# Kernel optimization log

Hardware: AMD Instinct MI355X
Metric: run time of the kernel (lower is better)

Reference implementation:

```python
import math
import jax, jax.numpy as jnp
import numpy as np

C = 1024  # n_embd
B, T = 4, 2048
H = 4 * C  # mlp hidden
EPS = 1e-5


def setup_inputs() -> dict:
    key = jax.random.key(0)
    ks = jax.random.split(key, 8)
    s = 0.02
    return {
        "x": jax.random.normal(ks[0], (B, T, C), jnp.float32),
        "ln1_g": jnp.ones((C,), jnp.float32),
        "ln1_b": jnp.zeros((C,), jnp.float32),
        "w_attn": jax.random.normal(ks[1], (C, 3 * C), jnp.float32) * s,
        "b_attn": jnp.zeros((3 * C,), jnp.float32),
        "w_proj": jax.random.normal(ks[2], (C, C), jnp.float32) * s,
        "b_proj": jnp.zeros((C,), jnp.float32),
        "ln2_g": jnp.ones((C,), jnp.float32),
        "ln2_b": jnp.zeros((C,), jnp.float32),
        "w_fc": jax.random.normal(ks[3], (C, H), jnp.float32) * s,
        "b_fc": jnp.zeros((H,), jnp.float32),
        "w_mlp_proj": jax.random.normal(ks[4], (H, C), jnp.float32) * s,
        "b_mlp_proj": jnp.zeros((C,), jnp.float32),
    }


def _layernorm(x, g, b):
    mu = jnp.mean(x, axis=-1, keepdims=True)
    var = jnp.mean(jnp.square(x - mu), axis=-1, keepdims=True)
    return (x - mu) * jax.lax.rsqrt(var + EPS) * g + b


def _new_gelu(x):
    c = math.sqrt(2.0 / math.pi)
    return 0.5 * x * (1.0 + jnp.tanh(c * (x + 0.044715 * x * x * x)))


def reference(x, ln1_g, ln1_b, w_attn, b_attn, w_proj, b_proj,
              ln2_g, ln2_b, w_fc, b_fc, w_mlp_proj, b_mlp_proj):
    # --- attention sublayer (single-head, full-dim, no causal mask) ---
    h = _layernorm(x, ln1_g, ln1_b)
    qkv = h @ w_attn + b_attn              # [B,T,3C]
    q, k, v = jnp.split(qkv, 3, axis=-1)   # each [B,T,C]
    scale = 1.0 / math.sqrt(C)
    att = jnp.einsum("btc,bsc->bts", q, k) * scale  # [B,T,T]
    att = jax.nn.softmax(att, axis=-1)
    y = jnp.einsum("bts,bsc->btc", att, v)
    y = y @ w_proj + b_proj
    x = x + y
    # --- MLP sublayer ---
    h2 = _layernorm(x, ln2_g, ln2_b)
    m = _new_gelu(h2 @ w_fc + b_fc) @ w_mlp_proj + b_mlp_proj
    return x + m
```

## Files before the change

kernel.cpp:

```cpp
#include <hip/hip_runtime.h>

typedef __bf16 bf16;
typedef bf16 bf16x8 __attribute__((ext_vector_type(8)));
typedef bf16 bf16x4 __attribute__((ext_vector_type(4)));
typedef float f32x4 __attribute__((ext_vector_type(4)));

#define C_DIM 1024
#define T_DIM 2048
#define B_DIM 4
#define H_DIM 4096

__device__ inline void gld_lds16(const bf16* g, bf16* l) {
    __builtin_amdgcn_global_load_lds(
        (const __attribute__((address_space(1))) unsigned int*)g,
        (__attribute__((address_space(3))) unsigned int*)l,
        16, 0, 0);
}

__device__ inline float fast_gelu(float u) {
    float k2 = 1.5957691216057308f * u + 0.07135480895843475f * u * u * u;
    float t = __expf(-k2);
    return u * __builtin_amdgcn_rcpf(1.0f + t);
}

template <int EPI, typename OutT, int BN>
__launch_bounds__(512, 2)
__global__ void gemm8p(const bf16* __restrict__ A, int lda, long long sA,
                       const bf16* __restrict__ Bt, int ldb, long long sB,
                       OutT* __restrict__ Cout, int ldc, long long sC,
                       const float* __restrict__ bias,
                       const float* __restrict__ resid, long long sR,
                       float alpha, int K) {
    constexpr int FN = BN / 64;
    constexpr int BQ = BN / 128;

    const int z = blockIdx.z;
    A += (long long)z * sA;
    Bt += (long long)z * sB;
    Cout += (long long)z * sC;
    if (resid) resid += (long long)z * sR;

    const int rowBase = blockIdx.x * 256;
    const int colBase = blockIdx.y * BN;

    __shared__ __align__(16) bf16 As[2 * 2 * 256 * 32];
    __shared__ __align__(16) bf16 Bs[2 * 2 * BN * 32];

    const int tid = threadIdx.x;
    const int w = tid >> 6;
    const int lane = tid & 63;
    const int wm = w >> 2, wn = w & 3;
    const int lr = lane & 15, lc = lane >> 4;

    const bf16* Ag = A + (size_t)(rowBase + (tid >> 2)) * lda + (tid & 3) * 8;
    const bf16* Bg = Bt + (size_t)(colBase + (tid >> 2)) * ldb + (tid & 3) * 8;
    const size_t ldaL = (size_t)lda, ldbL = (size_t)ldb;
    bf16* AsW = As + w * 512;
    bf16* BsW = Bs + w * 512;

    const int aBase = wm * 4096 + lr * 32 + lc * 8;
    const int bBase = wn * (FN * 512) + lr * 32 + lc * 8;

#define STAGE_A(buf, ks, tau) do {                                         \
        const bf16* _g = Ag + (size_t)(tau) * 64 + (ks) * 32;              \
        bf16* _l = AsW + ((buf) * 2 + (ks)) * 8192;                        \
        gld_lds16(_g, _l);                                                 \
        gld_lds16(_g + 128 * ldaL, _l + 4096);                             \
    } while (0)

#define STAGE_B(buf, ks, tau) do {                                         \
        const bf16* _g = Bg + (size_t)(tau) * 64 + (ks) * 32;              \
        bf16* _l = BsW + ((buf) * 2 + (ks)) * (BN * 32);                   \
        gld_lds16(_g, _l);                                                 \
        if constexpr (BQ == 2) gld_lds16(_g + 128 * ldbL, _l + 4096);      \
    } while (0)

#define LOAD_A(buf, ks, rh) do {                                           \
        _Pragma("unroll")                                                  \
        for (int i = 0; i < 4; i++)                                        \
            af[i] = *(const bf16x8*)(As + aBase + ((buf) * 2 + (ks)) * 8192 \
                                     + (rh) * 2048 + i * 512);             \
    } while (0)

#define LOAD_B(dst, buf, ks) do {                                          \
        _Pragma("unroll")                                                  \
        for (int j = 0; j < FN; j++)                                       \
            dst[j] = *(const bf16x8*)(Bs + bBase + ((buf) * 2 + (ks)) * (BN * 32) \
                                      + j * 512);                          \
    } while (0)

#define MMA(rh, bfr) do {                                                  \
        __builtin_amdgcn_s_setprio(1);                                     \
        _Pragma("unroll")                                                  \
        for (int i = 0; i < 4; i++)                                        \
            _Pragma("unroll")                                              \
            for (int j = 0; j < FN; j++)                                   \
                acc[(rh) * 4 + i][j] = __builtin_amdgcn_mfma_f32_16x16x32_bf16( \
                    af[i], bfr[j], acc[(rh) * 4 + i][j], 0, 0, 0);         \
        __builtin_amdgcn_s_setprio(0);                                     \
    } while (0)

#define BAR() do { __builtin_amdgcn_s_barrier(); __builtin_amdgcn_sched_barrier(0); } while (0)

#define VMW_STEADY() do {                                                  \
        if constexpr (BN == 256) asm volatile("s_waitcnt vmcnt(6)" ::: "memory"); \
        else                     asm volatile("s_waitcnt vmcnt(4)" ::: "memory"); \
    } while (0)
#define VMW0() asm volatile("s_waitcnt vmcnt(0)" ::: "memory")

    f32x4 acc[8][FN] = {};
    bf16x8 af[4], b0[FN], b1[FN];

    const int NT = K >> 6;

    STAGE_B(0, 0, 0);
    STAGE_A(0, 0, 0);
    STAGE_B(0, 1, 0);
    STAGE_A(0, 1, 0);
    STAGE_B(1, 0, 1);
    STAGE_A(1, 0, 1);
    STAGE_B(1, 1, 1);
    VMW_STEADY();
    BAR();

    for (int t = 0; t < NT; t += 2) {
        const bool more2 = (t + 2 < NT);

        LOAD_A(0, 0, 0); LOAD_B(b0, 0, 0);
        STAGE_A(1, 1, t + 1);
        BAR(); MMA(0, b0); BAR();
        LOAD_A(0, 0, 1);
        if (more2) STAGE_B(0, 0, t + 2);
        BAR(); MMA(1, b0); BAR();
        LOAD_A(0, 1, 0); LOAD_B(b1, 0, 1);
        if (more2) STAGE_A(0, 0, t + 2);
        BAR(); MMA(0, b1); BAR();
        LOAD_A(0, 1, 1);
        if (more2) STAGE_B(0, 1, t + 2);
        BAR(); MMA(1, b1);
        if (more2) VMW_STEADY(); else VMW0();
        BAR();

        LOAD_A(1, 0, 0); LOAD_B(b0, 1, 0);
        if (more2) STAGE_A(0, 1, t + 2);
        BAR(); MMA(0, b0); BAR();
        LOAD_A(1, 0, 1);
        if (more2) STAGE_B(1, 0, t + 3);
        BAR(); MMA(1, b0); BAR();
        LOAD_A(1, 1, 0); LOAD_B(b1, 1, 1);
        if (more2) STAGE_A(1, 0, t + 3);
        BAR(); MMA(0, b1); BAR();
        LOAD_A(1, 1, 1);
        if (more2) STAGE_B(1, 1, t + 3);
        BAR(); MMA(1, b1);
        if (more2) VMW_STEADY();
        BAR();
    }

#undef STAGE_A
#undef STAGE_B
#undef LOAD_A
#undef LOAD_B
#undef MMA
#undef BAR
#undef VMW_STEADY
#undef VMW0

    float bval[FN];
#pragma unroll
    for (int j = 0; j < FN; j++)
        bval[j] = bias ? bias[colBase + wn * (FN * 16) + j * 16 + lr] : 0.0f;

#pragma unroll
    for (int fi = 0; fi < 8; fi++) {
        const int row = rowBase + wm * 128 + fi * 16 + lc * 4;
#pragma unroll
        for (int fj = 0; fj < FN; fj++) {
            const int col = colBase + wn * (FN * 16) + fj * 16 + lr;
#pragma unroll
            for (int r = 0; r < 4; r++) {
                float v = acc[fi][fj][r] * alpha + bval[fj];
                if constexpr (EPI == 1) v = fast_gelu(v);
                if constexpr (EPI == 2) v += resid[(size_t)(row + r) * ldc + col];
                Cout[(size_t)(row + r) * ldc + col] = (OutT)v;
            }
        }
    }
}

__launch_bounds__(256)
__global__ void ln_kernel(const float* __restrict__ x, const float* __restrict__ g,
                          const float* __restrict__ b, bf16* __restrict__ out) {
    __shared__ float red[4];
    const int row = blockIdx.x;
    const int tid = threadIdx.x;
    const float4* xr = (const float4*)(x + (size_t)row * C_DIM);
    float4 v = xr[tid];
    float s = v.x + v.y + v.z + v.w;
#pragma unroll
    for (int m = 32; m; m >>= 1) s += __shfl_xor(s, m, 64);
    if ((tid & 63) == 0) red[tid >> 6] = s;
    __syncthreads();
    const float mu = (red[0] + red[1] + red[2] + red[3]) * (1.0f / C_DIM);
    const float dx = v.x - mu, dy = v.y - mu, dz = v.z - mu, dw = v.w - mu;
    float q = dx * dx + dy * dy + dz * dz + dw * dw;
#pragma unroll
    for (int m = 32; m; m >>= 1) q += __shfl_xor(q, m, 64);
    __syncthreads();
    if ((tid & 63) == 0) red[tid >> 6] = q;
    __syncthreads();
    const float var = (red[0] + red[1] + red[2] + red[3]) * (1.0f / C_DIM);
    const float rs = rsqrtf(var + 1e-5f);
    const float4 gg = ((const float4*)g)[tid];
    const float4 bb = ((const float4*)b)[tid];
    bf16x4 o;
    o[0] = (bf16)(dx * rs * gg.x + bb.x);
    o[1] = (bf16)(dy * rs * gg.y + bb.y);
    o[2] = (bf16)(dz * rs * gg.z + bb.z);
    o[3] = (bf16)(dw * rs * gg.w + bb.w);
    ((bf16x4*)(out + (size_t)row * C_DIM))[tid] = o;
}

__launch_bounds__(256)
__global__ void softmax_kernel(const bf16* __restrict__ S, bf16* __restrict__ P) {
    __shared__ float red[4];
    const size_t base = (size_t)blockIdx.x * T_DIM;
    const int tid = threadIdx.x;
    bf16x8 sv = ((const bf16x8*)(S + base))[tid];
    float e[8];
#pragma unroll
    for (int i = 0; i < 8; i++) e[i] = (float)sv[i];
    float mx = e[0];
#pragma unroll
    for (int i = 1; i < 8; i++) mx = fmaxf(mx, e[i]);
#pragma unroll
    for (int m = 32; m; m >>= 1) mx = fmaxf(mx, __shfl_xor(mx, m, 64));
    if ((tid & 63) == 0) red[tid >> 6] = mx;
    __syncthreads();
    mx = fmaxf(fmaxf(red[0], red[1]), fmaxf(red[2], red[3]));
    float s = 0.0f;
#pragma unroll
    for (int i = 0; i < 8; i++) {
        e[i] = __expf(e[i] - mx);
        s += e[i];
    }
#pragma unroll
    for (int m = 32; m; m >>= 1) s += __shfl_xor(s, m, 64);
    __syncthreads();
    if ((tid & 63) == 0) red[tid >> 6] = s;
    __syncthreads();
    const float inv = 1.0f / (red[0] + red[1] + red[2] + red[3]);
    bf16x8 p;
#pragma unroll
    for (int i = 0; i < 8; i++) p[i] = (bf16)(e[i] * inv);
    ((bf16x8*)(P + base))[tid] = p;
}

__global__ void transpose_f2b_all(const float* __restrict__ s0, bf16* __restrict__ d0,
                                  const float* __restrict__ s1, bf16* __restrict__ d1,
                                  const float* __restrict__ s2, bf16* __restrict__ d2,
                                  const float* __restrict__ s3, bf16* __restrict__ d3) {
    __shared__ float tile[32][33];
    int id = blockIdx.x;
    const float* src;
    bf16* dst;
    int R, Cc, local;
    if (id < 3072)       { src = s0; dst = d0; R = 1024; Cc = 3072; local = id; }
    else if (id < 4096)  { src = s1; dst = d1; R = 1024; Cc = 1024; local = id - 3072; }
    else if (id < 8192)  { src = s2; dst = d2; R = 1024; Cc = 4096; local = id - 4096; }
    else                 { src = s3; dst = d3; R = 4096; Cc = 1024; local = id - 8192; }
    const int tilesX = Cc >> 5;
    const int bx = (local % tilesX) * 32;
    const int by = (local / tilesX) * 32;
    const int tx = threadIdx.x, ty = threadIdx.y;
    for (int i = ty; i < 32; i += 8)
        tile[i][tx] = src[(size_t)(by + i) * Cc + bx + tx];
    __syncthreads();
    for (int i = ty; i < 32; i += 8)
        dst[(size_t)(bx + i) * R + by + tx] = (bf16)tile[tx][i];
}

__global__ void transpose_b2b(const bf16* __restrict__ src, int ldsrc, long long sstride,
                              bf16* __restrict__ dst, long long dstride, int R) {
    __shared__ bf16 tile[32][33];
    src += (long long)blockIdx.z * sstride;
    dst += (long long)blockIdx.z * dstride;
    const int bx = blockIdx.x * 32;
    const int by = blockIdx.y * 32;
    const int tx = threadIdx.x, ty = threadIdx.y;
    for (int i = ty; i < 32; i += 8)
        tile[i][tx] = src[(size_t)(by + i) * ldsrc + bx + tx];
    __syncthreads();
    for (int i = ty; i < 32; i += 8)
        dst[(size_t)(bx + i) * R + by + tx] = tile[tx][i];
}

extern "C" void kernel_launch(void* const* d_in, const int* in_sizes, int n_in,
                              void* d_out, int out_size, void* d_ws, size_t ws_size,
                              hipStream_t stream) {
    const float* x      = (const float*)d_in[0];
    const float* ln1_g  = (const float*)d_in[1];
    const float* ln1_b  = (const float*)d_in[2];
    const float* w_attn = (const float*)d_in[3];
    const float* b_attn = (const float*)d_in[4];
    const float* w_proj = (const float*)d_in[5];
    const float* b_proj = (const float*)d_in[6];
    const float* ln2_g  = (const float*)d_in[7];
    const float* ln2_b  = (const float*)d_in[8];
    const float* w_fc   = (const float*)d_in[9];
    const float* b_fc   = (const float*)d_in[10];
    const float* w_mlp  = (const float*)d_in[11];
    const float* b_mlp  = (const float*)d_in[12];
    float* out = (float*)d_out;

    const int M = B_DIM * T_DIM;

    char* base = (char*)d_ws;
    size_t off = 0;
    auto alloc = [&](size_t bytes) -> char* {
        char* p = base + off;
        off += (bytes + 255) & ~(size_t)255;
        return p;
    };
    bf16* wT_attn = (bf16*)alloc((size_t)3072 * 1024 * 2);
    bf16* wT_proj = (bf16*)alloc((size_t)1024 * 1024 * 2);
    bf16* wT_fc   = (bf16*)alloc((size_t)4096 * 1024 * 2);
    bf16* wT_mlp  = (bf16*)alloc((size_t)1024 * 4096 * 2);
    bf16* h       = (bf16*)alloc((size_t)M * 1024 * 2);
    bf16* qkv     = (bf16*)alloc((size_t)M * 3072 * 2);
    bf16* vT      = (bf16*)alloc((size_t)B_DIM * 1024 * 2048 * 2);
    bf16* S       = (bf16*)alloc((size_t)B_DIM * 2048 * 2048 * 2);
    bf16* P       = (bf16*)alloc((size_t)B_DIM * 2048 * 2048 * 2);
    bf16* y       = (bf16*)alloc((size_t)M * 1024 * 2);
    float* x2     = (float*)alloc((size_t)M * 1024 * 4);
    bf16* act     = (bf16*)S;

    const dim3 tb(32, 8);

    transpose_f2b_all<<<12288, tb, 0, stream>>>(w_attn, wT_attn, w_proj, wT_proj,
                                                w_fc, wT_fc, w_mlp, wT_mlp);

    ln_kernel<<<M, 256, 0, stream>>>(x, ln1_g, ln1_b, h);

    gemm8p<0, bf16, 128><<<dim3(32, 24, 1), 512, 0, stream>>>(
        h, 1024, 0, wT_attn, 1024, 0, qkv, 3072, 0, b_attn, nullptr, 0, 1.0f, 1024);

    transpose_b2b<<<dim3(1024 / 32, 2048 / 32, B_DIM), tb, 0, stream>>>(
        qkv + 2 * C_DIM, 3072, (long long)T_DIM * 3072, vT, (long long)C_DIM * T_DIM, T_DIM);

    gemm8p<0, bf16, 256><<<dim3(8, 8, B_DIM), 512, 0, stream>>>(
        qkv, 3072, (long long)T_DIM * 3072,
        qkv + C_DIM, 3072, (long long)T_DIM * 3072,
        S, 2048, (long long)T_DIM * T_DIM, nullptr, nullptr, 0, 0.03125f, 1024);

    softmax_kernel<<<B_DIM * T_DIM, 256, 0, stream>>>(S, P);

    gemm8p<0, bf16, 128><<<dim3(8, 8, B_DIM), 512, 0, stream>>>(
        P, 2048, (long long)T_DIM * T_DIM,
        vT, 2048, (long long)C_DIM * T_DIM,
        y, 1024, (long long)T_DIM * C_DIM, nullptr, nullptr, 0, 1.0f, 2048);

    gemm8p<2, float, 128><<<dim3(32, 8, 1), 512, 0, stream>>>(
        y, 1024, 0, wT_proj, 1024, 0, x2, 1024, 0, b_proj, x, 0, 1.0f, 1024);

    ln_kernel<<<M, 256, 0, stream>>>(x2, ln2_g, ln2_b, h);

    gemm8p<1, bf16, 256><<<dim3(32, 16, 1), 512, 0, stream>>>(
        h, 1024, 0, wT_fc, 1024, 0, act, 4096, 0, b_fc, nullptr, 0, 1.0f, 1024);

    gemm8p<2, float, 128><<<dim3(32, 8, 1), 512, 0, stream>>>(
        act, 4096, 0, wT_mlp, 4096, 0, out, 1024, 0, b_mlp, x2, 0, 1.0f, 4096);
}
```

Baseline: 534.1 us.

## Swizzle LDS chunks and remap BN=128 warps to a 4x2 grid

Adds an XOR swizzle on the 16-byte chunk index for both the global-to-LDS stores and the LDS fragment reads, aimed at removing LDS bank conflicts when loading MFMA operands. For the BN=128 variant, the warp layout changes from 2x4 to 4x2, so each warp computes a 64x64 tile (FM=4) instead of 128x32. That variant also gets its own pipelined main loop with matching vmcnt waits. This shifts the A and B reuse per warp in the smaller tile config, and the swizzle must stay consistent between writers and readers to remain correct.

After: 516.2 us. 1.03x faster.

```diff
diff --git a/kernel.cpp b/kernel.cpp
--- a/kernel.cpp
+++ b/kernel.cpp
@@ -31,8 +31,9 @@
                        const float* __restrict__ bias,
                        const float* __restrict__ resid, long long sR,
                        float alpha, int K) {
-    constexpr int FN = BN / 64;
     constexpr int BQ = BN / 128;
+    constexpr int FM = (BN == 256) ? 8 : 4;
+    constexpr int AW = (BN == 256) ? 128 : 64;
 
     const int z = blockIdx.z;
     A += (long long)z * sA;
@@ -49,17 +50,20 @@
     const int tid = threadIdx.x;
     const int w = tid >> 6;
     const int lane = tid & 63;
-    const int wm = w >> 2, wn = w & 3;
+    const int wm = (BN == 256) ? (w >> 2) : (w >> 1);
+    const int wn = (BN == 256) ? (w & 3) : (w & 1);
     const int lr = lane & 15, lc = lane >> 4;
 
-    const bf16* Ag = A + (size_t)(rowBase + (tid >> 2)) * lda + (tid & 3) * 8;
-    const bf16* Bg = Bt + (size_t)(colBase + (tid >> 2)) * ldb + (tid & 3) * 8;
+    const int gchunk = (tid & 3) ^ ((tid >> 3) & 3);
+    const bf16* Ag = A + (size_t)(rowBase + (tid >> 2)) * lda + gchunk * 8;
+    const bf16* Bg = Bt + (size_t)(colBase + (tid >> 2)) * ldb + gchunk * 8;
     const size_t ldaL = (size_t)lda, ldbL = (size_t)ldb;
     bf16* AsW = As + w * 512;
     bf16* BsW = Bs + w * 512;
 
-    const int aBase = wm * 4096 + lr * 32 + lc * 8;
-    const int bBase = wn * (FN * 512) + lr * 32 + lc * 8;
+    const int rchunk = lc ^ ((lr >> 1) & 3);
+    const int aBase = wm * (AW * 32) + lr * 32 + rchunk * 8;
+    const int bBase = wn * 2048 + lr * 32 + rchunk * 8;
 
 #define STAGE_A(buf, ks, tau) do {                                         \
         const bf16* _g = Ag + (size_t)(tau) * 64 + (ks) * 32;              \
@@ -84,7 +88,7 @@
 
 #define LOAD_B(dst, buf, ks) do {                                          \
         _Pragma("unroll")                                                  \
-        for (int j = 0; j < FN; j++)                                       \
+        for (int j = 0; j < 4; j++)                                        \
             dst[j] = *(const bf16x8*)(Bs + bBase + ((buf) * 2 + (ks)) * (BN * 32) \
                                       + j * 512);                          \
     } while (0)
@@ -94,67 +98,98 @@
         _Pragma("unroll")                                                  \
         for (int i = 0; i < 4; i++)                                        \
             _Pragma("unroll")                                              \
-            for (int j = 0; j < FN; j++)                                   \
+            for (int j = 0; j < 4; j++)                                    \
                 acc[(rh) * 4 + i][j] = __builtin_amdgcn_mfma_f32_16x16x32_bf16( \
                     af[i], bfr[j], acc[(rh) * 4 + i][j], 0, 0, 0);         \
         __builtin_amdgcn_s_setprio(0);                                     \
     } while (0)
 
 #define BAR() do { __builtin_amdgcn_s_barrier(); __builtin_amdgcn_sched_barrier(0); } while (0)
-
-#define VMW_STEADY() do {                                                  \
-        if constexpr (BN == 256) asm volatile("s_waitcnt vmcnt(6)" ::: "memory"); \
-        else                     asm volatile("s_waitcnt vmcnt(4)" ::: "memory"); \
-    } while (0)
-#define VMW0() asm volatile("s_waitcnt vmcnt(0)" ::: "memory")
-
-    f32x4 acc[8][FN] = {};
-    bf16x8 af[4], b0[FN], b1[FN];
+#define VMC(n) asm volatile("s_waitcnt vmcnt(" #n ")" ::: "memory")
+
+    f32x4 acc[FM][4] = {};
+    bf16x8 af[4], b0[4], b1[4];
 
     const int NT = K >> 6;
 
-    STAGE_B(0, 0, 0);
-    STAGE_A(0, 0, 0);
-    STAGE_B(0, 1, 0);
-    STAGE_A(0, 1, 0);
-    STAGE_B(1, 0, 1);
-    STAGE_A(1, 0, 1);
-    STAGE_B(1, 1, 1);
-    VMW_STEADY();
-    BAR();
-
-    for (int t = 0; t < NT; t += 2) {
-        const bool more2 = (t + 2 < NT);
-
-        LOAD_A(0, 0, 0); LOAD_B(b0, 0, 0);
-        STAGE_A(1, 1, t + 1);
-        BAR(); MMA(0, b0); BAR();
-        LOAD_A(0, 0, 1);
-        if (more2) STAGE_B(0, 0, t + 2);
-        BAR(); MMA(1, b0); BAR();
-        LOAD_A(0, 1, 0); LOAD_B(b1, 0, 1);
-        if (more2) STAGE_A(0, 0, t + 2);
-        BAR(); MMA(0, b1); BAR();
-        LOAD_A(0, 1, 1);
-        if (more2) STAGE_B(0, 1, t + 2);
-        BAR(); MMA(1, b1);
-        if (more2) VMW_STEADY(); else VMW0();
+    if constexpr (BN == 256) {
+        STAGE_B(0, 0, 0);
+        STAGE_A(0, 0, 0);
+        STAGE_B(0, 1, 0);
+        STAGE_A(0, 1, 0);
+        STAGE_B(1, 0, 1);
+        STAGE_A(1, 0, 1);
+        STAGE_B(1, 1, 1);
+        VMC(6);
         BAR();
 
-        LOAD_A(1, 0, 0); LOAD_B(b0, 1, 0);
-        if (more2) STAGE_A(0, 1, t + 2);
-        BAR(); MMA(0, b0); BAR();
-        LOAD_A(1, 0, 1);
-        if (more2) STAGE_B(1, 0, t + 3);
-        BAR(); MMA(1, b0); BAR();
-        LOAD_A(1, 1, 0); LOAD_B(b1, 1, 1);
-        if (more2) STAGE_A(1, 0, t + 3);
-        BAR(); MMA(0, b1); BAR();
-        LOAD_A(1, 1, 1);
-        if (more2) STAGE_B(1, 1, t + 3);
-        BAR(); MMA(1, b1);
-        if (more2) VMW_STEADY();
+        for (int t = 0; t < NT; t += 2) {
+            const bool more2 = (t + 2 < NT);
+            LOAD_A(0, 0, 0); LOAD_B(b0, 0, 0);
+            STAGE_A(1, 1, t + 1);
+            BAR(); MMA(0, b0); BAR();
+
+            LOAD_A(0, 0, 1);
+            if (more2) STAGE_B(0, 0, t + 2);
+            BAR(); MMA(1, b0); BAR();
+
+            LOAD_A(0, 1, 0); LOAD_B(b1, 0, 1);
+            if (more2) STAGE_A(0, 0, t + 2);
+            BAR(); MMA(0, b1); BAR();
+
+            LOAD_A(0, 1, 1);
+            if (more2) STAGE_B(0, 1, t + 2);
+            BAR(); MMA(1, b1);
+            if (more2) VMC(6); else VMC(0);
+            BAR();
+
+            LOAD_A(1, 0, 0); LOAD_B(b0, 1, 0);
+            if (more2) STAGE_A(0, 1, t + 2);
+            BAR(); MMA(0, b0); BAR();
+
+            LOAD_A(1, 0, 1);
+            if (more2) STAGE_B(1, 0, t + 3);
+            BAR(); MMA(1, b0); BAR();
+
+            LOAD_A(1, 1, 0); LOAD_B(b1, 1, 1);
+            if (more2) STAGE_A(1, 0, t + 3);
+            BAR(); MMA(0, b1); BAR();
+
+            LOAD_A(1, 1, 1);
+            if (more2) STAGE_B(1, 1, t + 3);
+            BAR(); MMA(1, b1);
+            if (more2) VMC(6);
+            BAR();
+        }
+    } else {
+        STAGE_A(0, 0, 0);
+        STAGE_B(0, 0, 0);
+        STAGE_A(0, 1, 0);
+        STAGE_B(0, 1, 0);
+        STAGE_A(1, 0, 1);
+        STAGE_B(1, 0, 1);
+        VMC(3);
         BAR();
+
+        for (int t = 0; t < NT; t += 2) {
+            const bool more2 = (t + 2 < NT);
+            LOAD_A(0, 0, 0); LOAD_B(b0, 0, 0);
+            STAGE_A(1, 1, t + 1); STAGE_B(1, 1, t + 1);
+            BAR(); MMA(0, b0); BAR();
+            LOAD_A(0, 1, 0); LOAD_B(b1, 0, 1);
+            if (more2) { STAGE_A(0, 0, t + 2); STAGE_B(0, 0, t + 2); }
+            BAR(); MMA(0, b1);
+            if (more2) VMC(3); else VMC(0);
+            BAR();
+            LOAD_A(1, 0, 0); LOAD_B(b0, 1, 0);
+            if (more2) { STAGE_A(0, 1, t + 2); STAGE_B(0, 1, t + 2); }
+            BAR(); MMA(0, b0); BAR();
+            LOAD_A(1, 1, 0); LOAD_B(b1, 1, 1);
+            if (more2) { STAGE_A(1, 0, t + 3); STAGE_B(1, 0, t + 3); }
+            BAR(); MMA(0, b1);
+            if (more2) VMC(3);
+            BAR();
+        }
     }
 
 #undef STAGE_A
@@ -163,20 +198,19 @@
 #undef LOAD_B
 #undef MMA
 #undef BAR
-#undef VMW_STEADY
-#undef VMW0
-
-    float bval[FN];
-#pragma unroll
-    for (int j = 0; j < FN; j++)
-        bval[j] = bias ? bias[colBase + wn * (FN * 16) + j * 16 + lr] : 0.0f;
-
-#pragma unroll
-    for (int fi = 0; fi < 8; fi++) {
-        const int row = rowBase + wm * 128 + fi * 16 + lc * 4;
-#pragma unroll
-        for (int fj = 0; fj < FN; fj++) {
-            const int col = colBase + wn * (FN * 16) + fj * 16 + lr;
+#undef VMC
+
+    float bval[4];
+#pragma unroll
+    for (int j = 0; j < 4; j++)
+        bval[j] = bias ? bias[colBase + wn * 64 + j * 16 + lr] : 0.0f;
+
+#pragma unroll
+    for (int fi = 0; fi < FM; fi++) {
+        const int row = rowBase + wm * AW + fi * 16 + lc * 4;
+#pragma unroll
+        for (int fj = 0; fj < 4; fj++) {
+            const int col = colBase + wn * 64 + fj * 16 + lr;
 #pragma unroll
             for (int r = 0; r < 4; r++) {
                 float v = acc[fi][fj][r] * alpha + bval[fj];
```
